# Kernel optimization log

Measured on AMD Instinct MI355X. Metric: run time of the kernel, lower is better.

Reference implementation:

```python
import jax, jax.numpy as jnp
import numpy as np
from jax import lax

B, C, H, W = 64, 3, 256, 256
E, D = 64, 32          # expert_nums, embed_dim
TOP_K = 2
NOISE_EPS = 0.01
ALPHA = 0.8


def setup_inputs() -> dict:
    key = jax.random.key(0)
    ks = jax.random.split(key, 16)
    n = lambda k, shape, s=0.05: jax.random.normal(k, shape, jnp.float32) * s
    return {
        "task_id": jax.random.randint(ks[0], (B,), 0, 10),
        "degradation_info": jax.random.normal(ks[1], (B, C, H, W), jnp.float32),
        "noise": jax.random.normal(ks[2], (B, E), jnp.float32),
        "mlp_w1": n(ks[3], (1, D)), "mlp_b1": jnp.zeros((D,), jnp.float32),
        "mlp_w2": n(ks[4], (D, D)), "mlp_b2": jnp.zeros((D,), jnp.float32),
        "conv1_w": n(ks[5], (16, C, 3, 3)), "conv1_b": jnp.zeros((16,), jnp.float32),
        "conv2_w": n(ks[6], (32, 16, 3, 3)), "conv2_b": jnp.zeros((32,), jnp.float32),
        "deg_w": n(ks[7], (32, D)), "deg_b": jnp.zeros((D,), jnp.float32),
        "expert_keys": jax.random.normal(ks[8], (E, D), jnp.float32),
        "gate_w": n(ks[9], (E, E)), "gate_b": jnp.zeros((E,), jnp.float32),
        "noise_w": n(ks[10], (E, E)), "noise_b": jnp.zeros((E,), jnp.float32),
    }


def _conv(x, w):
    return lax.conv_general_dilated(
        x, w, window_strides=(1, 1), padding="SAME",
        dimension_numbers=("NCHW", "OIHW", "NCHW"))


def reference(task_id, degradation_info, noise,
              mlp_w1, mlp_b1, mlp_w2, mlp_b2,
              conv1_w, conv1_b, conv2_w, conv2_b,
              deg_w, deg_b, expert_keys,
              gate_w, gate_b, noise_w, noise_b):
    # task embedding: Linear(1,D) -> ReLU -> Linear(D,D)
    t = task_id.astype(jnp.float32)[:, None]                       # [B,1]
    task_embed = jax.nn.relu(t @ mlp_w1 + mlp_b1) @ mlp_w2 + mlp_b2  # [B,D]

    # degradation conv embed: conv->relu->conv->relu->global avg pool
    h = jax.nn.relu(_conv(degradation_info, conv1_w) + conv1_b[None, :, None, None])
    h = jax.nn.relu(_conv(h, conv2_w) + conv2_b[None, :, None, None])
    feat = h.mean(axis=(2, 3))                                     # [B,32]
    deg_embed = feat @ deg_w + deg_b                               # [B,D]

    combined = task_embed + (1.0 - ALPHA) * deg_embed              # [B,D]
    sim = combined @ expert_keys.T / jnp.sqrt(jnp.float32(D))      # [B,E]
    expert_weight = jax.nn.softmax(sim, axis=1)

    clean_logits = expert_weight @ gate_w + gate_b                 # [B,E]
    stddev = jax.nn.softplus(expert_weight @ noise_w + noise_b) + NOISE_EPS
    logits = clean_logits + noise * stddev                         # train=True path

    top_logits, top_idx = lax.top_k(logits, min(TOP_K + 1, E))
    tk_logits = top_logits[:, :TOP_K]                              # [B,k]
    tk_idx = top_idx[:, :TOP_K]
    tk_gates = jax.nn.softmax(tk_logits, axis=1)

    rows = jnp.arange(logits.shape[0])[:, None]
    gates = jnp.zeros_like(logits).at[rows, tk_idx].set(tk_gates)  # scatter
    load = gates.sum(axis=0)                                       # [E]
    return gates, load
```

## Files before the change

kernel.cpp:

```cpp
#include <hip/hip_runtime.h>
#include <math.h>

typedef __attribute__((ext_vector_type(8)))  short  short8;
typedef __attribute__((ext_vector_type(4)))  short  svec4;
typedef __attribute__((ext_vector_type(4)))  float  floatx4;
typedef __attribute__((ext_vector_type(16))) float  floatx16;
typedef __attribute__((ext_vector_type(2)))  unsigned uintx2;

__device__ __forceinline__ short bf16rne(float f) {
    unsigned u = __float_as_uint(f);
    unsigned r = (u + 0x7FFFu + ((u >> 16) & 1u)) >> 16;
    return (short)r;
}
__device__ __forceinline__ unsigned pk2(float a, float b) {
#if __has_builtin(__builtin_amdgcn_cvt_pk_bf16_f32)
    auto t = __builtin_amdgcn_cvt_pk_bf16_f32(a, b);
    unsigned u; __builtin_memcpy(&u, &t, 4); return u;
#else
    return (unsigned)(unsigned short)bf16rne(a) |
           ((unsigned)(unsigned short)bf16rne(b) << 16);
#endif
}

#define WS_FRAG_OFF  8192
#define WS_BIAS1_OFF (WS_FRAG_OFF + 11 * 64 * 16)
#define WS_BIAS2_OFF (WS_BIAS1_OFF + 64 * 16)

__global__ __launch_bounds__(256) void build_frags_kernel(
    const float* __restrict__ w1,
    const float* __restrict__ b1,
    const float* __restrict__ w2,
    const float* __restrict__ b2,
    void* __restrict__ ws,
    float* __restrict__ out)
{
    const int t = threadIdx.x;
    float* feat = (float*)ws;
    for (int i = t; i < 2048; i += 256) feat[i] = 0.0f;
    if (t >= 64 && t < 128) out[4096 + (t - 64)] = 0.0f;

    if (t < 64) {
        const int lane = t;
        const int q = lane >> 4, ml = lane & 15;
        const int n32 = lane & 31, half = lane >> 5;
        short8* F = (short8*)((char*)ws + WS_FRAG_OFF);

        short8 W1a;
#pragma unroll
        for (int j = 0; j < 8; ++j) {
            int p = q * 2 + (j >> 2), c = j & 3;
            W1a[j] = (c < 3) ? bf16rne(w1[ml * 27 + c * 9 + p]) : (short)0;
        }
        F[0 * 64 + lane] = W1a;

        short8 W1b;
#pragma unroll
        for (int j = 0; j < 8; ++j) {
            W1b[j] = (q == 0 && j < 3) ? bf16rne(w1[ml * 27 + j * 9 + 8])
                                       : (short)0;
        }
        F[1 * 64 + lane] = W1b;

#pragma unroll
        for (int s = 0; s < 9; ++s) {
            short8 Bs;
#pragma unroll
            for (int j = 0; j < 8; ++j) {
                int ic = half * 8 + j;
                Bs[j] = bf16rne(w2[(n32 * 16 + ic) * 9 + s]);
            }
            F[(2 + s) * 64 + lane] = Bs;
        }
        floatx4 bv;
#pragma unroll
        for (int r = 0; r < 4; ++r) bv[r] = b1[q * 4 + r];
        ((floatx4*)((char*)ws + WS_BIAS1_OFF))[lane] = bv;
        ((float*)((char*)ws + WS_BIAS2_OFF))[lane] = b2[n32];
    }
}

__device__ __forceinline__ void conv1_tile(
    short* __restrict__ s_h1, const short* __restrict__ s_in4,
    const int* lcB, int basePixByte, int wIdx, bool valid, bool wmask,
    short8 W1a, short8 W1b, floatx4 biasv)
{
    const char* base = (const char*)s_in4 + basePixByte;
    svec4 r0 = *(const svec4*)(base + lcB[0]);
    svec4 r1 = *(const svec4*)(base + lcB[1]);
    svec4 r2 = *(const svec4*)(base + lcB[2]);
    short8 Bx, By;
    Bx[0]=r0[0]; Bx[1]=r0[1]; Bx[2]=r0[2]; Bx[3]=r0[3];
    Bx[4]=r1[0]; Bx[5]=r1[1]; Bx[6]=r1[2]; Bx[7]=r1[3];
    By[0]=r2[0]; By[1]=r2[1]; By[2]=r2[2]; By[3]=r2[3];
    By[4]=r2[0]; By[5]=r2[1]; By[6]=r2[2]; By[7]=r2[3];
    floatx4 acc = biasv;
    acc = __builtin_amdgcn_mfma_f32_16x16x32_bf16(W1a, Bx, acc, 0, 0, 0);
    acc = __builtin_amdgcn_mfma_f32_16x16x32_bf16(W1b, By, acc, 0, 0, 0);
    float v0 = fmaxf(acc[0], 0.f), v1 = fmaxf(acc[1], 0.f);
    float v2 = fmaxf(acc[2], 0.f), v3 = fmaxf(acc[3], 0.f);
    if (!valid) { v0 = 0.f; v1 = 0.f; v2 = 0.f; v3 = 0.f; }
    if (wmask) {
        uintx2 w; w.x = pk2(v0, v1); w.y = pk2(v2, v3);
        *(uintx2*)&s_h1[wIdx] = w;
    }
}

__global__ __launch_bounds__(256, 6) void conv_feat_kernel(
    const float* __restrict__ x,
    const void*  __restrict__ ws_ro,
    float* __restrict__ feat_sum)
{
    __shared__ short s_in4[20 * 20 * 4];
    __shared__ short s_h1[324 * 24];
    __shared__ float s_part[4][32];

    const int t    = threadIdx.x;
    const int lane = t & 63, wv = t >> 6;
    const int q    = lane >> 4, ml = lane & 15;
    const int n32  = lane & 31, half = lane >> 5;
    const int tx = blockIdx.x, ty = blockIdx.y, b = blockIdx.z;
    const bool border = (tx == 0) | (tx == 15) | (ty == 0) | (ty == 15);

    const short8* F = (const short8*)((const char*)ws_ro + WS_FRAG_OFF);
    short8 W1a = F[0 * 64 + lane];
    short8 W1b = F[1 * 64 + lane];
    short8 B2[9];
#pragma unroll
    for (int s = 0; s < 9; ++s) B2[s] = F[(2 + s) * 64 + lane];
    floatx4 biasv = ((const floatx4*)((const char*)ws_ro + WS_BIAS1_OFF))[lane];
    float   b2v   = ((const float*)((const char*)ws_ro + WS_BIAS2_OFF))[lane];

    int lcB[3];
    {
        int p0 = q * 2, p1 = q * 2 + 1;
        lcB[0] = ((p0 / 3) * 20 + p0 % 3) * 8;
        lcB[1] = ((p1 / 3) * 20 + p1 % 3) * 8;
        lcB[2] = (2 * 20 + 2) * 8;
    }

    const int gy0 = ty * 16 - 2, gx0 = tx * 16 - 2;
    const float* xb = x + (size_t)b * 3 * 65536;
    if (!border) {
        for (int i = t; i < 400; i += 256) {
            int r = i / 20, col = i % 20;
            const float* p = xb + (gy0 + r) * 256 + (gx0 + col);
            float v0 = p[0], v1 = p[65536], v2 = p[131072];
            uintx2 w; w.x = pk2(v0, v1); w.y = pk2(v2, 0.f);
            *(uintx2*)&s_in4[i * 4] = w;
        }
    } else {
        for (int i = t; i < 400; i += 256) {
            int r = i / 20, col = i % 20;
            int gy = gy0 + r, gx = gx0 + col;
            float v0 = 0.f, v1 = 0.f, v2 = 0.f;
            if ((unsigned)gy < 256u && (unsigned)gx < 256u) {
                const float* p = xb + gy * 256 + gx;
                v0 = p[0]; v1 = p[65536]; v2 = p[131072];
            }
            uintx2 w; w.x = pk2(v0, v1); w.y = pk2(v2, 0.f);
            *(uintx2*)&s_in4[i * 4] = w;
        }
    }
    __syncthreads();

    const int mlb = ml * 8;
    const int wbase = ml * 24 + q * 4;
    if (!border) {
#pragma unroll
        for (int i = 0; i < 4; ++i) {
            int tile = wv + 4 * i;
            conv1_tile(s_h1, s_in4, lcB, tile * 160 + mlb,
                       tile * 432 + wbase, true, true, W1a, W1b, biasv);
        }
        if (wv < 2) {
            int tile = wv + 16;
            conv1_tile(s_h1, s_in4, lcB, tile * 160 + mlb,
                       tile * 432 + wbase, true, true, W1a, W1b, biasv);
        } else {
            int cc = wv - 2;
            conv1_tile(s_h1, s_in4, lcB, ml * 160 + (16 + cc) * 8,
                       (ml * 18 + 16 + cc) * 24 + q * 4, true, true,
                       W1a, W1b, biasv);
        }
        if (wv == 0) {
            int ml2 = ml & 3;
            int iy = 16 + (ml2 >> 1), ix = 16 + (ml2 & 1);
            conv1_tile(s_h1, s_in4, lcB, iy * 160 + ix * 8,
                       (iy * 18 + ix) * 24 + q * 4, true, ml < 4,
                       W1a, W1b, biasv);
        }
    } else {
        const bool gxOK = (unsigned)(tx * 16 - 1 + ml) < 256u;
#pragma unroll
        for (int i = 0; i < 4; ++i) {
            int tile = wv + 4 * i;
            bool ok = ((unsigned)(ty * 16 - 1 + tile) < 256u) & gxOK;
            conv1_tile(s_h1, s_in4, lcB, tile * 160 + mlb,
                       tile * 432 + wbase, ok, true, W1a, W1b, biasv);
        }
        if (wv < 2) {
            int tile = wv + 16;
            bool ok = ((unsigned)(ty * 16 - 1 + tile) < 256u) & gxOK;
            conv1_tile(s_h1, s_in4, lcB, tile * 160 + mlb,
                       tile * 432 + wbase, ok, true, W1a, W1b, biasv);
        } else {
            int cc = wv - 2;
            bool ok = ((unsigned)(ty * 16 - 1 + ml) < 256u) &
                      ((unsigned)(tx * 16 + 15 + cc) < 256u);
            conv1_tile(s_h1, s_in4, lcB, ml * 160 + (16 + cc) * 8,
                       (ml * 18 + 16 + cc) * 24 + q * 4, ok, true,
                       W1a, W1b, biasv);
        }
        if (wv == 0) {
            int ml2 = ml & 3;
            int iy = 16 + (ml2 >> 1), ix = 16 + (ml2 & 1);
            bool ok = ((unsigned)(ty * 16 - 1 + iy) < 256u) &
                      ((unsigned)(tx * 16 - 1 + ix) < 256u);
            conv1_tile(s_h1, s_in4, lcB, iy * 160 + ix * 8,
                       (iy * 18 + ix) * 24 + q * 4, ok, ml < 4,
                       W1a, W1b, biasv);
        }
    }
    __syncthreads();

    float part = 0.0f;
    const int prow0 = (n32 >> 4), pcol = n32 & 15;
#pragma unroll
    for (int tt = 0; tt < 2; ++tt) {
        int pix0 = (2 * (2 * wv + tt) + prow0) * 18 + pcol;
        const short* A0 = s_h1 + pix0 * 24 + half * 8;
        floatx16 acc;
#pragma unroll
        for (int r = 0; r < 16; ++r) acc[r] = b2v;
#pragma unroll
        for (int s = 0; s < 9; ++s) {
            const int ky = s / 3, kx = s % 3;
            short8 Ax = *(const short8*)(A0 + (ky * 18 + kx) * 24);
            acc = __builtin_amdgcn_mfma_f32_32x32x16_bf16(Ax, B2[s], acc, 0, 0, 0);
        }
#pragma unroll
        for (int r = 0; r < 16; ++r) part += fmaxf(acc[r], 0.0f);
    }
    part += __shfl_xor(part, 32);
    if (lane < 32) s_part[wv][n32] = part;
    __syncthreads();
    if (t < 32) {
        float ssum = s_part[0][t] + s_part[1][t] + s_part[2][t] + s_part[3][t];
        atomicAdd(feat_sum + b * 32 + t, ssum);
    }
}

__global__ __launch_bounds__(64) void router_gate_kernel(
    const int* __restrict__ task_id,
    const float* __restrict__ noise,
    const float* __restrict__ mlp_w1,
    const float* __restrict__ mlp_b1,
    const float* __restrict__ mlp_w2,
    const float* __restrict__ mlp_b2,
    const float* __restrict__ deg_w,
    const float* __restrict__ deg_b,
    const float* __restrict__ keys,
    const float* __restrict__ gate_w,
    const float* __restrict__ gate_b,
    const float* __restrict__ noise_w,
    const float* __restrict__ noise_b,
    const float* __restrict__ feat_sum,
    float* __restrict__ out)
{
    const int b = blockIdx.x;
    const int e = threadIdx.x;

    __shared__ float s_te[32];
    __shared__ float s_comb[32];
    __shared__ float s_ew[64];

    if (e < 32) {
        float tf = (float)task_id[b];
        s_te[e] = fmaxf(tf * mlp_w1[e] + mlp_b1[e], 0.0f);
    }
    __syncthreads();
    if (e < 32) {
        float acc = mlp_b2[e];
        for (int k = 0; k < 32; ++k) acc += s_te[k] * mlp_w2[k * 32 + e];
        float dacc = deg_b[e];
        for (int c = 0; c < 32; ++c)
            dacc += (feat_sum[b * 32 + c] * (1.0f / 65536.0f)) * deg_w[c * 32 + e];
        s_comb[e] = acc + 0.2f * dacc;
    }
    __syncthreads();

    float s = 0.0f;
    for (int d = 0; d < 32; ++d) s += s_comb[d] * keys[e * 32 + d];
    s *= 0.17677669529663687f;

    float m = s;
    for (int off = 32; off; off >>= 1) m = fmaxf(m, __shfl_xor(m, off));
    float p = expf(s - m);
    float sum = p;
    for (int off = 32; off; off >>= 1) sum += __shfl_xor(sum, off);
    float w = p / sum;
    s_ew[e] = w;
    __syncthreads();

    float cl = gate_b[e], nz = noise_b[e];
    for (int k = 0; k < 64; ++k) {
        float ewk = s_ew[k];
        cl += ewk * gate_w[k * 64 + e];
        nz += ewk * noise_w[k * 64 + e];
    }
    float sp = (nz > 20.0f) ? nz : log1pf(expf(nz));
    float logit = cl + noise[b * 64 + e] * (sp + 0.01f);

    float v0 = logit; int i0 = e;
    for (int off = 32; off; off >>= 1) {
        float ov = __shfl_xor(v0, off);
        int   oi = __shfl_xor(i0, off);
        if (ov > v0 || (ov == v0 && oi < i0)) { v0 = ov; i0 = oi; }
    }
    float v1 = (e == i0) ? -INFINITY : logit; int i1 = e;
    for (int off = 32; off; off >>= 1) {
        float ov = __shfl_xor(v1, off);
        int   oi = __shfl_xor(i1, off);
        if (ov > v1 || (ov == v1 && oi < i1)) { v1 = ov; i1 = oi; }
    }

    float e1 = expf(v1 - v0);
    float g0 = 1.0f / (1.0f + e1);
    float g1 = e1 / (1.0f + e1);

    float g = (e == i0) ? g0 : (e == i1) ? g1 : 0.0f;
    out[b * 64 + e] = g;
    if (g != 0.0f) atomicAdd(out + 64 * 64 + e, g);
}

extern "C" void kernel_launch(void* const* d_in, const int* in_sizes, int n_in,
                              void* d_out, int out_size, void* d_ws, size_t ws_size,
                              hipStream_t stream) {
    const int*   task_id = (const int*)d_in[0];
    const float* x       = (const float*)d_in[1];
    const float* noise   = (const float*)d_in[2];
    const float* mlp_w1  = (const float*)d_in[3];
    const float* mlp_b1  = (const float*)d_in[4];
    const float* mlp_w2  = (const float*)d_in[5];
    const float* mlp_b2  = (const float*)d_in[6];
    const float* conv1_w = (const float*)d_in[7];
    const float* conv1_b = (const float*)d_in[8];
    const float* conv2_w = (const float*)d_in[9];
    const float* conv2_b = (const float*)d_in[10];
    const float* deg_w   = (const float*)d_in[11];
    const float* deg_b   = (const float*)d_in[12];
    const float* keys    = (const float*)d_in[13];
    const float* gate_w  = (const float*)d_in[14];
    const float* gate_b  = (const float*)d_in[15];
    const float* noise_w = (const float*)d_in[16];
    const float* noise_b = (const float*)d_in[17];

    float* out  = (float*)d_out;
    float* feat = (float*)d_ws;

    build_frags_kernel<<<1, 256, 0, stream>>>(conv1_w, conv1_b, conv2_w,
                                              conv2_b, d_ws, out);
    dim3 gridA(16, 16, 64);
    conv_feat_kernel<<<gridA, 256, 0, stream>>>(x, d_ws, feat);
    router_gate_kernel<<<64, 64, 0, stream>>>(
        task_id, noise, mlp_w1, mlp_b1, mlp_w2, mlp_b2, deg_w, deg_b, keys,
        gate_w, gate_b, noise_w, noise_b, feat, out);
}
```

Baseline: 182.7 us.

## Enlarge conv tile to 32x32 with planar h1 layout and register-rotated A fragments

Each block of the fused conv kernel now covers a 32x32 output tile instead of 16x16, so the grid shrinks to 8x8x64. This cuts the halo overhead of reloading and recomputing conv1 on border pixels. The conv1 output is stored in shared memory as two channel-half planes, and conv2 keeps a 3x3 window of A fragments in registers that rotates down the rows, reusing rows across iterations instead of reloading all nine. In exchange, shared memory per block grows and the launch bound drops to 3 blocks per CU, which lowers occupancy and may expose more latency.

```diff
diff --git a/kernel.cpp b/kernel.cpp
--- a/kernel.cpp
+++ b/kernel.cpp
@@ -25,6 +25,8 @@
 #define WS_FRAG_OFF  8192
 #define WS_BIAS1_OFF (WS_FRAG_OFF + 11 * 64 * 16)
 #define WS_BIAS2_OFF (WS_BIAS1_OFF + 64 * 16)
+
+#define PLANE_B 18496
 
 __global__ __launch_bounds__(256) void build_frags_kernel(
     const float* __restrict__ w1,
@@ -80,14 +82,13 @@
 }
 
 __device__ __forceinline__ void conv1_tile(
-    short* __restrict__ s_h1, const short* __restrict__ s_in4,
-    const int* lcB, int basePixByte, int wIdx, bool valid, bool wmask,
+    char* __restrict__ wptr, const char* __restrict__ inb,
+    const int* lcB, int gbyte, int wbyte, bool valid, bool wmask,
     short8 W1a, short8 W1b, floatx4 biasv)
 {
-    const char* base = (const char*)s_in4 + basePixByte;
-    svec4 r0 = *(const svec4*)(base + lcB[0]);
-    svec4 r1 = *(const svec4*)(base + lcB[1]);
-    svec4 r2 = *(const svec4*)(base + lcB[2]);
+    svec4 r0 = *(const svec4*)(inb + gbyte + lcB[0]);
+    svec4 r1 = *(const svec4*)(inb + gbyte + lcB[1]);
+    svec4 r2 = *(const svec4*)(inb + gbyte + lcB[2]);
     short8 Bx, By;
     Bx[0]=r0[0]; Bx[1]=r0[1]; Bx[2]=r0[2]; Bx[3]=r0[3];
     Bx[4]=r1[0]; Bx[5]=r1[1]; Bx[6]=r1[2]; Bx[7]=r1[3];
@@ -101,17 +102,17 @@
     if (!valid) { v0 = 0.f; v1 = 0.f; v2 = 0.f; v3 = 0.f; }
     if (wmask) {
         uintx2 w; w.x = pk2(v0, v1); w.y = pk2(v2, v3);
-        *(uintx2*)&s_h1[wIdx] = w;
-    }
-}
-
-__global__ __launch_bounds__(256, 6) void conv_feat_kernel(
+        *(uintx2*)(wptr + wbyte) = w;
+    }
+}
+
+__global__ __launch_bounds__(256, 3) void conv_feat_kernel(
     const float* __restrict__ x,
     const void*  __restrict__ ws_ro,
     float* __restrict__ feat_sum)
 {
-    __shared__ short s_in4[20 * 20 * 4];
-    __shared__ short s_h1[324 * 24];
+    __shared__ short s_in4[36 * 36 * 4];
+    __shared__ short s_h1[2 * 9248];
     __shared__ float s_part[4][32];
 
     const int t    = threadIdx.x;
@@ -119,7 +120,7 @@
     const int q    = lane >> 4, ml = lane & 15;
     const int n32  = lane & 31, half = lane >> 5;
     const int tx = blockIdx.x, ty = blockIdx.y, b = blockIdx.z;
-    const bool border = (tx == 0) | (tx == 15) | (ty == 0) | (ty == 15);
+    const bool border = (tx == 0) | (tx == 7) | (ty == 0) | (ty == 7);
 
     const short8* F = (const short8*)((const char*)ws_ro + WS_FRAG_OFF);
     short8 W1a = F[0 * 64 + lane];
@@ -133,25 +134,25 @@
     int lcB[3];
     {
         int p0 = q * 2, p1 = q * 2 + 1;
-        lcB[0] = ((p0 / 3) * 20 + p0 % 3) * 8;
-        lcB[1] = ((p1 / 3) * 20 + p1 % 3) * 8;
-        lcB[2] = (2 * 20 + 2) * 8;
-    }
-
-    const int gy0 = ty * 16 - 2, gx0 = tx * 16 - 2;
+        lcB[0] = ((p0 / 3) * 36 + p0 % 3) * 8;
+        lcB[1] = ((p1 / 3) * 36 + p1 % 3) * 8;
+        lcB[2] = (2 * 36 + 2) * 8;
+    }
+
+    const int gy0 = ty * 32 - 2, gx0 = tx * 32 - 2;
     const float* xb = x + (size_t)b * 3 * 65536;
     if (!border) {
-        for (int i = t; i < 400; i += 256) {
-            int r = i / 20, col = i % 20;
-            const float* p = xb + (gy0 + r) * 256 + (gx0 + col);
+        for (int i = t; i < 1296; i += 256) {
+            int r = i / 36, c = i - r * 36;
+            const float* p = xb + (gy0 + r) * 256 + gx0 + c;
             float v0 = p[0], v1 = p[65536], v2 = p[131072];
             uintx2 w; w.x = pk2(v0, v1); w.y = pk2(v2, 0.f);
             *(uintx2*)&s_in4[i * 4] = w;
         }
     } else {
-        for (int i = t; i < 400; i += 256) {
-            int r = i / 20, col = i % 20;
-            int gy = gy0 + r, gx = gx0 + col;
+        for (int i = t; i < 1296; i += 256) {
+            int r = i / 36, c = i - r * 36;
+            int gy = gy0 + r, gx = gx0 + c;
             float v0 = 0.f, v1 = 0.f, v2 = 0.f;
             if ((unsigned)gy < 256u && (unsigned)gx < 256u) {
                 const float* p = xb + gy * 256 + gx;
@@ -163,83 +164,98 @@
     }
     __syncthreads();
 
-    const int mlb = ml * 8;
-    const int wbase = ml * 24 + q * 4;
+    char* wptr = (char*)s_h1 + (q >> 1) * PLANE_B + (q & 1) * 8;
+    const char* inb = (const char*)s_in4;
+    const int mlb = ml * 8, ml16 = ml * 16;
     if (!border) {
 #pragma unroll
-        for (int i = 0; i < 4; ++i) {
-            int tile = wv + 4 * i;
-            conv1_tile(s_h1, s_in4, lcB, tile * 160 + mlb,
-                       tile * 432 + wbase, true, true, W1a, W1b, biasv);
-        }
-        if (wv < 2) {
-            int tile = wv + 16;
-            conv1_tile(s_h1, s_in4, lcB, tile * 160 + mlb,
-                       tile * 432 + wbase, true, true, W1a, W1b, biasv);
-        } else {
-            int cc = wv - 2;
-            conv1_tile(s_h1, s_in4, lcB, ml * 160 + (16 + cc) * 8,
-                       (ml * 18 + 16 + cc) * 24 + q * 4, true, true,
+        for (int i = 0; i < 17; ++i) {
+            int u = wv * 17 + i, row = u >> 1, ch = u & 1;
+            conv1_tile(wptr, inb, lcB, row * 288 + ch * 128 + mlb,
+                       row * 544 + ch * 256 + ml16, true, true,
+                       W1a, W1b, biasv);
+        }
+        {
+            int col = 32 + (wv >> 1), rb = (wv & 1) * 16;
+            conv1_tile(wptr, inb, lcB, (rb + ml) * 288 + col * 8,
+                       ml * 544 + (rb * 34 + col) * 16, true, true,
                        W1a, W1b, biasv);
         }
         if (wv == 0) {
             int ml2 = ml & 3;
-            int iy = 16 + (ml2 >> 1), ix = 16 + (ml2 & 1);
-            conv1_tile(s_h1, s_in4, lcB, iy * 160 + ix * 8,
-                       (iy * 18 + ix) * 24 + q * 4, true, ml < 4,
+            int iy = 32 + (ml2 >> 1), ix = 32 + (ml2 & 1);
+            conv1_tile(wptr, inb, lcB, iy * 288 + ix * 8,
+                       (iy * 34 + ix) * 16, true, ml < 4, W1a, W1b, biasv);
+        }
+    } else {
+        const bool gxOK0 = (unsigned)(tx * 32 - 1 + ml) < 256u;
+        const bool gxOK1 = (unsigned)(tx * 32 + 15 + ml) < 256u;
+#pragma unroll
+        for (int i = 0; i < 17; ++i) {
+            int u = wv * 17 + i, row = u >> 1, ch = u & 1;
+            bool ok = ((unsigned)(ty * 32 - 1 + row) < 256u) &
+                      (ch ? gxOK1 : gxOK0);
+            conv1_tile(wptr, inb, lcB, row * 288 + ch * 128 + mlb,
+                       row * 544 + ch * 256 + ml16, ok, true,
                        W1a, W1b, biasv);
         }
-    } else {
-        const bool gxOK = (unsigned)(tx * 16 - 1 + ml) < 256u;
-#pragma unroll
-        for (int i = 0; i < 4; ++i) {
-            int tile = wv + 4 * i;
-            bool ok = ((unsigned)(ty * 16 - 1 + tile) < 256u) & gxOK;
-            conv1_tile(s_h1, s_in4, lcB, tile * 160 + mlb,
-                       tile * 432 + wbase, ok, true, W1a, W1b, biasv);
-        }
-        if (wv < 2) {
-            int tile = wv + 16;
-            bool ok = ((unsigned)(ty * 16 - 1 + tile) < 256u) & gxOK;
-            conv1_tile(s_h1, s_in4, lcB, tile * 160 + mlb,
-                       tile * 432 + wbase, ok, true, W1a, W1b, biasv);
-        } else {
-            int cc = wv - 2;
-            bool ok = ((unsigned)(ty * 16 - 1 + ml) < 256u) &
-                      ((unsigned)(tx * 16 + 15 + cc) < 256u);
-            conv1_tile(s_h1, s_in4, lcB, ml * 160 + (16 + cc) * 8,
-                       (ml * 18 + 16 + cc) * 24 + q * 4, ok, true,
+        {
+            int col = 32 + (wv >> 1), rb = (wv & 1) * 16;
+            bool ok = ((unsigned)(ty * 32 - 1 + rb + ml) < 256u) &
+                      ((unsigned)(tx * 32 - 1 + col) < 256u);
+            conv1_tile(wptr, inb, lcB, (rb + ml) * 288 + col * 8,
+                       ml * 544 + (rb * 34 + col) * 16, ok, true,
                        W1a, W1b, biasv);
         }
         if (wv == 0) {
             int ml2 = ml & 3;
-            int iy = 16 + (ml2 >> 1), ix = 16 + (ml2 & 1);
-            bool ok = ((unsigned)(ty * 16 - 1 + iy) < 256u) &
-                      ((unsigned)(tx * 16 - 1 + ix) < 256u);
-            conv1_tile(s_h1, s_in4, lcB, iy * 160 + ix * 8,
-                       (iy * 18 + ix) * 24 + q * 4, ok, ml < 4,
-                       W1a, W1b, biasv);
+            int iy = 32 + (ml2 >> 1), ix = 32 + (ml2 & 1);
+            bool ok = ((unsigned)(ty * 32 - 1 + iy) < 256u) &
+                      ((unsigned)(tx * 32 - 1 + ix) < 256u);
+            conv1_tile(wptr, inb, lcB, iy * 288 + ix * 8,
+                       (iy * 34 + ix) * 16, ok, ml < 4, W1a, W1b, biasv);
         }
     }
     __syncthreads();
 
     float part = 0.0f;
-    const int prow0 = (n32 >> 4), pcol = n32 & 15;
-#pragma unroll
-    for (int tt = 0; tt < 2; ++tt) {
-        int pix0 = (2 * (2 * wv + tt) + prow0) * 18 + pcol;
-        const short* A0 = s_h1 + pix0 * 24 + half * 8;
-        floatx16 acc;
-#pragma unroll
-        for (int r = 0; r < 16; ++r) acc[r] = b2v;
-#pragma unroll
-        for (int s = 0; s < 9; ++s) {
-            const int ky = s / 3, kx = s % 3;
-            short8 Ax = *(const short8*)(A0 + (ky * 18 + kx) * 24);
-            acc = __builtin_amdgcn_mfma_f32_32x32x16_bf16(Ax, B2[s], acc, 0, 0, 0);
-        }
-#pragma unroll
-        for (int r = 0; r < 16; ++r) part += fmaxf(acc[r], 0.0f);
+    {
+        const int prow0 = n32 >> 4, pcol = n32 & 15;
+        const int ch = wv >> 1, tp0 = (wv & 1) * 8;
+        const int ox = ch * 16 + pcol;
+        const char* pl = (const char*)s_h1 + half * PLANE_B;
+        int pb = ((2 * tp0 + prow0) * 34 + ox) * 16;
+        short8 Af[3][3];
+#pragma unroll
+        for (int ky = 0; ky < 3; ++ky)
+#pragma unroll
+            for (int kx = 0; kx < 3; ++kx)
+                Af[ky][kx] = *(const short8*)(pl + pb + (ky * 34 + kx) * 16);
+#pragma unroll
+        for (int it = 0; it < 8; ++it) {
+            const int rb = (2 * it) % 3;
+            floatx16 acc;
+#pragma unroll
+            for (int r = 0; r < 16; ++r) acc[r] = b2v;
+#pragma unroll
+            for (int s = 0; s < 9; ++s) {
+                const int ky = s / 3, kx = s % 3;
+                acc = __builtin_amdgcn_mfma_f32_32x32x16_bf16(
+                        Af[(rb + ky) % 3][kx], B2[s], acc, 0, 0, 0);
+            }
+#pragma unroll
+            for (int r = 0; r < 16; ++r) part += fmaxf(acc[r], 0.0f);
+            if (it < 7) {
+                pb += 1088;
+#pragma unroll
+                for (int kx = 0; kx < 3; ++kx) {
+                    Af[rb][kx] =
+                        *(const short8*)(pl + pb + (1 * 34 + kx) * 16);
+                    Af[(rb + 1) % 3][kx] =
+                        *(const short8*)(pl + pb + (2 * 34 + kx) * 16);
+                }
+            }
+        }
     }
     part += __shfl_xor(part, 32);
     if (lane < 32) s_part[wv][n32] = part;
@@ -360,7 +376,7 @@
 
     build_frags_kernel<<<1, 256, 0, stream>>>(conv1_w, conv1_b, conv2_w,
                                               conv2_b, d_ws, out);
-    dim3 gridA(16, 16, 64);
+    dim3 gridA(8, 8, 64);
     conv_feat_kernel<<<gridA, 256, 0, stream>>>(x, d_ws, feat);
     router_gate_kernel<<<64, 64, 0, stream>>>(
         task_id, noise, mlp_w1, mlp_b1, mlp_w2, mlp_b2, deg_w, deg_b, keys,
```

Result: faster. 174.1 us (-4.7%).
